# Kernel optimization log

Hardware: AMD Instinct MI355X
Metric: run time of the kernel (lower is better)

The kernel has to match this reference:

```python
import jax, jax.numpy as jnp
import numpy as np

B, T, D, H, L, V = 64, 512, 1024, 512, 2, 32000
RESET = 32  # hidden state zeroed every 32 steps (ei > 0 and ei % 32 == 0)


def setup_inputs() -> dict:
    key = jax.random.key(0)
    ks = jax.random.split(key, 10)
    s = 1.0 / np.sqrt(H)
    u = lambda k, shp: jax.random.uniform(k, shp, jnp.float32, -s, s)
    return {
        'rt': jax.random.randint(ks[0], (B, T), 0, V),
        're': jax.random.randint(ks[1], (B, T), 0, V),
        'rm': jax.random.randint(ks[2], (B, T), 0, V),
        'h0': jnp.zeros((L, 2, B, H), jnp.float32),
        'c0': jnp.zeros((L, 2, B, H), jnp.float32),
        'E_rt': jax.random.normal(ks[3], (V, D), jnp.float32) * 0.02,
        'E_re': jax.random.normal(ks[4], (V, D), jnp.float32) * 0.02,
        'E_rm': jax.random.normal(ks[5], (V, D), jnp.float32) * 0.02,
        'Wih': u(ks[6], (L, 2, 4 * H, D)),
        'Whh': u(ks[7], (L, 2, 4 * H, H)),
        'bih': u(ks[8], (L, 2, 4 * H)),
        'bhh': u(ks[9], (L, 2, 4 * H)),
    }


def _lstm_scan(x_seq, h0, c0, Wih, Whh, bih, bhh):
    # x_seq: [T, B, D]; h0/c0: [L, 2, B, H]
    bias = (bih + bhh)[:, :, None, :]  # [L, 2, 1, 4H]

    def step(carry, inp):
        h, c = carry
        x, t = inp
        reset = jnp.logical_and(t > 0, t % RESET == 0)
        h = jnp.where(reset, 0.0, h)
        c = jnp.where(reset, 0.0, c)
        new_h, new_c = [], []
        layer_in = x  # [B, D]
        for l in range(L):
            # both directions step forward in time (faithful to per-step bilstm call)
            g = (jnp.einsum('bd,xgd->xbg', layer_in, Wih[l])
                 + jnp.einsum('xbh,xgh->xbg', h[l], Whh[l])
                 + bias[l])  # [2, B, 4H]
            i, f, gg, o = jnp.split(g, 4, axis=-1)  # PyTorch gate order i,f,g,o
            cc = jax.nn.sigmoid(f) * c[l] + jax.nn.sigmoid(i) * jnp.tanh(gg)
            hh = jax.nn.sigmoid(o) * jnp.tanh(cc)
            new_h.append(hh)
            new_c.append(cc)
            layer_in = jnp.concatenate([hh[0], hh[1]], axis=-1)  # [B, 2H] = [B, D]
        return (jnp.stack(new_h), jnp.stack(new_c)), layer_in

    (hT, cT), out = jax.lax.scan(step, (h0, c0), (x_seq, jnp.arange(x_seq.shape[0])))
    return out, hT, cT  # out: [T, B, D]


def reference(rt, re, rm, h0, c0, E_rt, E_re, E_rm, Wih, Whh, bih, bhh):
    emb = E_rt[rt] + E_re[re] + E_rm[rm]  # [B, T, D]
    out, hT, cT = _lstm_scan(jnp.transpose(emb, (1, 0, 2)), h0, c0, Wih, Whh, bih, bhh)
    outputs = jnp.transpose(out, (1, 0, 2))  # [B, T, D]
    hidden = (hT.reshape(L * 2, B, H), cT.reshape(L * 2, B, H))
    return outputs, hidden
```

## Files before the change

### kernel.cpp

```cpp
#include <hip/hip_runtime.h>
#include <hip/hip_bf16.h>
#include <stdint.h>


typedef _Float16 half8 __attribute__((ext_vector_type(8)));
typedef _Float16 half4v __attribute__((ext_vector_type(4)));
typedef float float4v __attribute__((ext_vector_type(4)));

#define AS1C(p) ((const __attribute__((address_space(1))) void*)(p))
#define AS3(p)  ((__attribute__((address_space(3))) void*)(p))

__device__ __forceinline__ float sigm(float x){ return 1.0f/(1.0f + __expf(-x)); }
__device__ __forceinline__ float tanh_f(float x){ return 2.0f/(1.0f + __expf(-2.0f*x)) - 1.0f; }

__global__ __launch_bounds__(256) void k_embed(
    const int* __restrict__ rt, const int* __restrict__ re, const int* __restrict__ rm,
    const float* __restrict__ Ert, const float* __restrict__ Ere, const float* __restrict__ Erm,
    _Float16* __restrict__ emb)
{
  size_t idx = (size_t)blockIdx.x * 256 + threadIdx.x;
  int dq = (int)(idx & 255);
  size_t bt = idx >> 8;
  int b = (int)(bt >> 9);
  int t = (int)(bt & 511);
  int irt = rt[bt], ire = re[bt], irm = rm[bt];
  float4 v0 = ((const float4*)Ert)[(size_t)irt * 256 + dq];
  float4 v1 = ((const float4*)Ere)[(size_t)ire * 256 + dq];
  float4 v2 = ((const float4*)Erm)[(size_t)irm * 256 + dq];
  half4v h;
  h[0] = (_Float16)(v0.x + v1.x + v2.x);
  h[1] = (_Float16)(v0.y + v1.y + v2.y);
  h[2] = (_Float16)(v0.z + v1.z + v2.z);
  h[3] = (_Float16)(v0.w + v1.w + v2.w);
  ((half4v*)emb)[((size_t)t * 64 + b) * 256 + dq] = h;
}

__global__ __launch_bounds__(256) void k_prepw(
    const float* __restrict__ Wih, const float* __restrict__ Whh,
    _Float16* __restrict__ Wc)
{
  int bid = blockIdx.x;
  int ld = bid >> 11;
  int n  = bid & 2047;
  int g  = (n >> 4) & 3;
  int j  = ((n >> 6) << 4) | (n & 15);
  int srow = g * 512 + j;
  const float* sx = Wih + ((size_t)ld * 2048 + srow) * 1024;
  const float* sh = Whh + ((size_t)ld * 2048 + srow) * 512;
  _Float16* dst = Wc + ((size_t)ld * 2048 + n) * 1536;
  for (int k = threadIdx.x; k < 1536; k += 256)
    dst[k] = (_Float16)(k < 1024 ? sx[k] : sh[k - 1024]);
}

__global__ __launch_bounds__(256) void k_prepb(
    const float* __restrict__ bih, const float* __restrict__ bhh,
    float* __restrict__ biasc)
{
  int idx = blockIdx.x * 256 + threadIdx.x;
  int ld = idx >> 11, n = idx & 2047;
  int g = (n >> 4) & 3;
  int j = ((n >> 6) << 4) | (n & 15);
  int srow = ld * 2048 + g * 512 + j;
  biasc[idx] = bih[srow] + bhh[srow];
}

__global__ __launch_bounds__(256) void k_init(
    int layer, const float* __restrict__ h0, const float* __restrict__ c0,
    _Float16* __restrict__ hbuf, float* __restrict__ cbuf)
{
  int idx = blockIdx.x * 256 + threadIdx.x;
  int dir = idx >> 19;
  int rj = idx & ((1 << 19) - 1);
  int r = rj >> 9, j = rj & 511;
  float hv = 0.f, cv = 0.f;
  if (r < 64) {
    size_t s0 = ((size_t)(layer * 2 + dir) * 64 + r) * 512 + j;
    hv = h0[s0]; cv = c0[s0];
  }
  hbuf[idx] = (_Float16)hv;
  cbuf[idx] = cv;
}

__global__ __launch_bounds__(512, 4) void k_step(
    int s0, int s1,
    const _Float16* __restrict__ emb,
    _Float16* __restrict__ out0,
    float* __restrict__ outs,
    _Float16* __restrict__ hbAll,
    float* __restrict__ cbAll,
    const _Float16* __restrict__ Wc,
    const float* __restrict__ biasc,
    float* __restrict__ hT, float* __restrict__ cT)
{
  const int layer = blockIdx.z;
  const int s = layer ? s1 : s0;
  if ((unsigned)s > 31u) return;

  const _Float16* xsrc = layer ? out0 : emb;
  const _Float16* hin  = hbAll + ((size_t)(layer * 2 + (s & 1))) * 1048576;
  _Float16*       hout = hbAll + ((size_t)(layer * 2 + ((s & 1) ^ 1))) * 1048576;
  float*          cbuf = cbAll + (size_t)layer * 1048576;

  __shared__ __align__(16) _Float16 smem[32768];
  const int tid = threadIdx.x;
  const int w = tid >> 6, l = tid & 63;
  const int nb = blockIdx.x;
  const int m0 = blockIdx.y * 128;
  const int dir = nb >> 4;
  const int n0 = (nb & 15) * 128;
  const int ld = layer * 2 + dir;

  const char* pX[4]; const char* pH[4]; uint32_t ldsoff[4];
  #pragma unroll
  for (int ii = 0; ii < 4; ++ii) {
    int instr = w * 4 + ii;
    if (instr < 16) {
      int c = instr * 64 + l;
      int row = c & 127, kc = c >> 7;
      int r = m0 + row;
      int erow = ((r >> 6) * 32 + s) * 64 + (r & 63);
      pX[ii] = (const char*)(xsrc + (size_t)erow * 1024 + kc * 8);
      pH[ii] = (const char*)(hin + ((size_t)dir * 1024 + r) * 512 + kc * 8) - 2048;
      ldsoff[ii] = (uint32_t)instr * 1024u;
    } else {
      int c = (instr - 16) * 64 + l;
      int nl = c & 127, kc = c >> 7;
      const char* p = (const char*)(Wc + ((size_t)ld * 2048 + n0 + nl) * 1536 + kc * 8);
      pX[ii] = p; pH[ii] = p;
      ldsoff[ii] = 16384u + (uint32_t)(instr - 16) * 1024u;
    }
  }

  const int wm = w >> 1, wn = w & 1;
  float4v acc[2][4];
  const float4v vzero = {0.f, 0.f, 0.f, 0.f};
  #pragma unroll
  for (int mf = 0; mf < 2; ++mf)
    #pragma unroll
    for (int nf = 0; nf < 4; ++nf) acc[mf][nf] = vzero;

  auto stage = [&](int it, int buf) {
    const int k0 = it * 64;
    const bool isx = (it < 16);
    #pragma unroll
    for (int ii = 0; ii < 4; ++ii) {
      const char* src = (isx ? pX[ii] : pH[ii]) + (size_t)k0 * 2;
      __builtin_amdgcn_global_load_lds(AS1C(src),
          AS3(((char*)smem) + (size_t)buf * 32768 + ldsoff[ii]), 16, 0, 0);
    }
  };

  stage(0, 0);
  __syncthreads();
  #pragma unroll 2
  for (int it = 0; it < 24; ++it) {
    const int cur = it & 1;
    if (it + 1 < 24) stage(it + 1, cur ^ 1);
    const _Float16* sA = smem + (size_t)cur * 16384;
    const _Float16* sB = sA + 8192;
    #pragma unroll
    for (int kk = 0; kk < 64; kk += 32) {
      const int kcb = (kk >> 3) + (l >> 4);
      half8 a[2], b[4];
      #pragma unroll
      for (int mf = 0; mf < 2; ++mf)
        a[mf] = *(const half8*)(sA + ((size_t)kcb * 128 + wm * 32 + mf * 16 + (l & 15)) * 8);
      #pragma unroll
      for (int nf = 0; nf < 4; ++nf)
        b[nf] = *(const half8*)(sB + ((size_t)kcb * 128 + wn * 64 + nf * 16 + (l & 15)) * 8);
      #pragma unroll
      for (int mf = 0; mf < 2; ++mf)
        #pragma unroll
        for (int nf = 0; nf < 4; ++nf)
          acc[mf][nf] = __builtin_amdgcn_mfma_f32_16x16x32_f16(a[mf], b[nf], acc[mf][nf], 0, 0, 0);
    }
    __syncthreads();
  }

  const int q = (nb & 15) * 2 + wn;
  const int jj = l & 15;
  const int j = q * 16 + jj;
  const int bb_base = ld * 2048 + n0 + wn * 64;
  const float bias_i = biasc[bb_base + 0 * 16 + jj];
  const float bias_f = biasc[bb_base + 1 * 16 + jj];
  const float bias_g = biasc[bb_base + 2 * 16 + jj];
  const float bias_o = biasc[bb_base + 3 * 16 + jj];

  #pragma unroll
  for (int mf = 0; mf < 2; ++mf) {
    #pragma unroll
    for (int reg = 0; reg < 4; ++reg) {
      int r = m0 + wm * 32 + mf * 16 + (l >> 4) * 4 + reg;
      float ip = acc[mf][0][reg] + bias_i;
      float fp = acc[mf][1][reg] + bias_f;
      float gp = acc[mf][2][reg] + bias_g;
      float op = acc[mf][3][reg] + bias_o;
      size_t cidx = ((size_t)dir * 1024 + r) * 512 + j;
      float cold = cbuf[cidx];
      float cn = sigm(fp) * cold + sigm(ip) * tanh_f(gp);
      float hn = sigm(op) * tanh_f(cn);
      cbuf[cidx] = cn;
      hout[cidx] = (_Float16)hn;
      int chunk = r >> 6, bb = r & 63;
      int t = chunk * 32 + s;
      if (layer == 0) {
        out0[((size_t)t * 64 + bb) * 1024 + dir * 512 + j] = (_Float16)hn;
      } else {
        outs[((size_t)bb * 512 + t) * 1024 + dir * 512 + j] = hn;
      }
      if (s == 31 && chunk == 15) {
        size_t hidx = ((size_t)(layer * 2 + dir) * 64 + bb) * 512 + j;
        hT[hidx] = hn; cT[hidx] = cn;
      }
    }
  }
}

extern "C" void kernel_launch(void* const* d_in, const int* in_sizes, int n_in,
                              void* d_out, int out_size, void* d_ws, size_t ws_size,
                              hipStream_t stream)
{
  const int*   rt  = (const int*)d_in[0];
  const int*   re  = (const int*)d_in[1];
  const int*   rm  = (const int*)d_in[2];
  const float* h0  = (const float*)d_in[3];
  const float* c0  = (const float*)d_in[4];
  const float* Ert = (const float*)d_in[5];
  const float* Ere = (const float*)d_in[6];
  const float* Erm = (const float*)d_in[7];
  const float* Wih = (const float*)d_in[8];
  const float* Whh = (const float*)d_in[9];
  const float* bih = (const float*)d_in[10];
  const float* bhh = (const float*)d_in[11];

  float* outs = (float*)d_out;
  float* hT = outs + (size_t)64 * 512 * 1024;
  float* cT = hT + (size_t)4 * 64 * 512;

  char* p = (char*)d_ws;
  _Float16* emb  = (_Float16*)p;  p += (size_t)32768 * 1024 * 2;
  _Float16* out0 = (_Float16*)p;  p += (size_t)32768 * 1024 * 2;
  _Float16* Wc   = (_Float16*)p;  p += (size_t)4 * 2048 * 1536 * 2;
  float*    biasc= (float*)p;     p += (size_t)4 * 2048 * 4;
  _Float16* hbAll= (_Float16*)p;  p += (size_t)4 * 1048576 * 2;
  float*    cbAll= (float*)p;     p += (size_t)2 * 1048576 * 4;

  k_prepw<<<8192, 256, 0, stream>>>(Wih, Whh, Wc);
  k_prepb<<<32, 256, 0, stream>>>(bih, bhh, biasc);
  k_embed<<<32768, 256, 0, stream>>>(rt, re, rm, Ert, Ere, Erm, emb);
  k_init<<<4096, 256, 0, stream>>>(0, h0, c0, hbAll, cbAll);
  k_init<<<4096, 256, 0, stream>>>(1, h0, c0, hbAll + (size_t)2 * 1048576,
                                   cbAll + (size_t)1048576);

  for (int k = 0; k < 33; ++k) {
    k_step<<<dim3(32, 8, 2), 512, 0, stream>>>(k, k - 1, emb, out0, outs,
                                               hbAll, cbAll, Wc, biasc, hT, cT);
  }
}
```

Before: 2.279 ms.

## Overlap next-tile loads with MFMA via vmcnt waits and raw barriers

The step GEMM loop replaces the __syncthreads pairs with explicit s_waitcnt vmcnt(4) after issuing the next stage's global-to-LDS loads, plus raw s_barrier calls fenced by sched_barrier and s_setprio around the MFMA block. This lets the prefetch for the next K-tile stay in flight while the current tile is consumed, instead of draining all memory ops at each sync. Separately, the embedding kernel now handles two batch rows per thread with half the blocks, which raises memory-level parallelism. The hand-written waitcnt counts depend on each thread issuing exactly four loads per stage, and any mismatch would break correctness.

```diff
diff --git a/kernel.cpp b/kernel.cpp
--- a/kernel.cpp
+++ b/kernel.cpp
@@ -21,18 +21,27 @@
   size_t idx = (size_t)blockIdx.x * 256 + threadIdx.x;
   int dq = (int)(idx & 255);
   size_t bt = idx >> 8;
-  int b = (int)(bt >> 9);
-  int t = (int)(bt & 511);
-  int irt = rt[bt], ire = re[bt], irm = rm[bt];
-  float4 v0 = ((const float4*)Ert)[(size_t)irt * 256 + dq];
-  float4 v1 = ((const float4*)Ere)[(size_t)ire * 256 + dq];
-  float4 v2 = ((const float4*)Erm)[(size_t)irm * 256 + dq];
-  half4v h;
-  h[0] = (_Float16)(v0.x + v1.x + v2.x);
-  h[1] = (_Float16)(v0.y + v1.y + v2.y);
-  h[2] = (_Float16)(v0.z + v1.z + v2.z);
-  h[3] = (_Float16)(v0.w + v1.w + v2.w);
-  ((half4v*)emb)[((size_t)t * 64 + b) * 256 + dq] = h;
+  size_t bt2 = bt + 16384;
+  int a0 = rt[bt],  a1 = re[bt],  a2 = rm[bt];
+  int b0 = rt[bt2], b1 = re[bt2], b2 = rm[bt2];
+  float4 u0 = ((const float4*)Ert)[(size_t)a0 * 256 + dq];
+  float4 u1 = ((const float4*)Ere)[(size_t)a1 * 256 + dq];
+  float4 u2 = ((const float4*)Erm)[(size_t)a2 * 256 + dq];
+  float4 w0 = ((const float4*)Ert)[(size_t)b0 * 256 + dq];
+  float4 w1 = ((const float4*)Ere)[(size_t)b1 * 256 + dq];
+  float4 w2 = ((const float4*)Erm)[(size_t)b2 * 256 + dq];
+  half4v h, g;
+  h[0] = (_Float16)(u0.x + u1.x + u2.x);
+  h[1] = (_Float16)(u0.y + u1.y + u2.y);
+  h[2] = (_Float16)(u0.z + u1.z + u2.z);
+  h[3] = (_Float16)(u0.w + u1.w + u2.w);
+  g[0] = (_Float16)(w0.x + w1.x + w2.x);
+  g[1] = (_Float16)(w0.y + w1.y + w2.y);
+  g[2] = (_Float16)(w0.z + w1.z + w2.z);
+  g[3] = (_Float16)(w0.w + w1.w + w2.w);
+  int b_ = (int)(bt >> 9), t_ = (int)(bt & 511);
+  ((half4v*)emb)[((size_t)t_ * 64 + b_) * 256 + dq] = h;
+  ((half4v*)emb)[((size_t)t_ * 64 + (b_ + 32)) * 256 + dq] = g;
 }
 
 __global__ __launch_bounds__(256) void k_prepw(
@@ -95,7 +104,6 @@
   const int layer = blockIdx.z;
   const int s = layer ? s1 : s0;
   if ((unsigned)s > 31u) return;
-
   const _Float16* xsrc = layer ? out0 : emb;
   const _Float16* hin  = hbAll + ((size_t)(layer * 2 + (s & 1))) * 1048576;
   _Float16*       hout = hbAll + ((size_t)(layer * 2 + ((s & 1) ^ 1))) * 1048576;
@@ -151,13 +159,22 @@
   };
 
   stage(0, 0);
-  __syncthreads();
   #pragma unroll 2
   for (int it = 0; it < 24; ++it) {
     const int cur = it & 1;
-    if (it + 1 < 24) stage(it + 1, cur ^ 1);
+    if (it < 23) {
+      stage(it + 1, cur ^ 1);
+      asm volatile("s_waitcnt vmcnt(4)" ::: "memory");
+    } else {
+      asm volatile("s_waitcnt vmcnt(0)" ::: "memory");
+    }
+    __builtin_amdgcn_sched_barrier(0);
+    __builtin_amdgcn_s_barrier();
+    __builtin_amdgcn_sched_barrier(0);
+
     const _Float16* sA = smem + (size_t)cur * 16384;
     const _Float16* sB = sA + 8192;
+    __builtin_amdgcn_s_setprio(1);
     #pragma unroll
     for (int kk = 0; kk < 64; kk += 32) {
       const int kcb = (kk >> 3) + (l >> 4);
@@ -174,7 +191,11 @@
         for (int nf = 0; nf < 4; ++nf)
           acc[mf][nf] = __builtin_amdgcn_mfma_f32_16x16x32_f16(a[mf], b[nf], acc[mf][nf], 0, 0, 0);
     }
-    __syncthreads();
+    __builtin_amdgcn_s_setprio(0);
+    asm volatile("s_waitcnt lgkmcnt(0)" ::: "memory");
+    __builtin_amdgcn_sched_barrier(0);
+    __builtin_amdgcn_s_barrier();
+    __builtin_amdgcn_sched_barrier(0);
   }
 
   const int q = (nb & 15) * 2 + wn;
@@ -247,7 +268,7 @@
 
   k_prepw<<<8192, 256, 0, stream>>>(Wih, Whh, Wc);
   k_prepb<<<32, 256, 0, stream>>>(bih, bhh, biasc);
-  k_embed<<<32768, 256, 0, stream>>>(rt, re, rm, Ert, Ere, Erm, emb);
+  k_embed<<<16384, 256, 0, stream>>>(rt, re, rm, Ert, Ere, Erm, emb);
   k_init<<<4096, 256, 0, stream>>>(0, h0, c0, hbAll, cbAll);
   k_init<<<4096, 256, 0, stream>>>(1, h0, c0, hbAll + (size_t)2 * 1048576,
                                    cbAll + (size_t)1048576);
```

After: 2.254 ms. No clear change (-1.1%).
